# Kernel optimization log

Hardware: AMD Instinct MI355X
Metric: run time of the kernel (lower is better)

Reference implementation:

```python
import jax, jax.numpy as jnp
import numpy as np


def setup_inputs() -> dict:
    key = jax.random.key(0)
    ks = jax.random.split(key, 10)
    B, T = 256, 256
    num_q, dk, dv, C = 1000, 128, 128, 32
    xn_k = (2.0 / (dk + C)) ** 0.5   # xavier_normal for Mk
    xn_v = (2.0 / (C + dv)) ** 0.5   # xavier_normal for Mv
    return dict(
        skills=jax.random.randint(ks[0], (B, T), 0, num_q),
        responses=jax.random.randint(ks[1], (B, T), 0, 2),
        k_emb=jax.random.normal(ks[2], (num_q, dk), dtype=jnp.float32) * 0.05,
        v_emb=jax.random.normal(ks[3], (2 * num_q, dv), dtype=jnp.float32) * 0.05,
        Mk=jax.random.normal(ks[4], (dk, C), dtype=jnp.float32) * xn_k,
        Mv0=jax.random.normal(ks[5], (C, dv), dtype=jnp.float32) * xn_v,
        f_W=jax.random.normal(ks[6], (2 * dk, dk), dtype=jnp.float32) * 0.05,
        f_b=jnp.zeros((dk,), jnp.float32),
        p_W=jax.random.normal(ks[7], (dk, 1), dtype=jnp.float32) * 0.05,
        p_b=jnp.zeros((1,), jnp.float32),
        e_W=jax.random.normal(ks[8], (dv, dv), dtype=jnp.float32) * 0.05,
        e_b=jnp.zeros((dv,), jnp.float32),
        a_W=jax.random.normal(ks[9], (dv, dv), dtype=jnp.float32) * 0.05,
        a_b=jnp.zeros((dv,), jnp.float32),
    )


def reference(skills, responses, k_emb, v_emb, Mk, Mv0, f_W, f_b,
              p_W, p_b, e_W, e_b, a_W, a_b):
    num_q = k_emb.shape[0]
    B = skills.shape[0]
    masked_r = responses * (responses > -1).astype(responses.dtype)
    qr = skills + num_q * masked_r
    kt_all = k_emb[skills]   # (B, T, dk)
    vt_all = v_emb[qr]       # (B, T, dv)
    Mvt0 = jnp.broadcast_to(Mv0[None], (B,) + Mv0.shape)  # (B, C, dv)

    def step(Mvt, xs):
        kt, vt = xs                                      # (B,dk), (B,dv)
        wt = jax.nn.softmax(kt @ Mk, axis=-1)            # (B, C) read weights
        rt = jnp.einsum('bc,bcd->bd', wt, Mvt)           # memory read
        ft = jnp.tanh(jnp.concatenate([rt, kt], axis=-1) @ f_W + f_b)
        pt = jax.nn.sigmoid(ft @ p_W + p_b)[:, 0]        # (B,)
        et = jax.nn.sigmoid(vt @ e_W + e_b)              # erase gate
        at = jnp.tanh(vt @ a_W + a_b)                    # add vector
        Mvt = Mvt * (1.0 - wt[:, :, None] * et[:, None, :]) \
              + wt[:, :, None] * at[:, None, :]
        return Mvt, pt

    xs = (jnp.swapaxes(kt_all, 0, 1), jnp.swapaxes(vt_all, 0, 1))  # time-major
    _, p = jax.lax.scan(step, Mvt0, xs)                  # (T, B)
    p = jnp.swapaxes(p, 0, 1)                            # (B, T)
    pred = p[:, :-1]
    true = responses[:, 1:].astype(jnp.float32)
    return pred, true
```

## Files before the change

kernel.cpp:

```cpp
#include <hip/hip_runtime.h>
#include <math.h>

#define BB 256
#define TT 256
#define NQ 1000
#define DK 128
#define DV 128
#define CC 32

typedef short s16x8 __attribute__((ext_vector_type(8)));
typedef float f32x4 __attribute__((ext_vector_type(4)));
typedef float f32x2 __attribute__((ext_vector_type(2)));

__device__ __forceinline__ float fast_sigmoid(float x) {
    x = fminf(fmaxf(x, -30.f), 30.f);
    return 1.f / (1.f + __expf(-x));
}
__device__ __forceinline__ float fast_tanh(float x) {
    x = fminf(fmaxf(x, -15.f), 15.f);
    float t = __expf(2.f * x);
    return (t - 1.f) / (t + 1.f);
}
__device__ __forceinline__ unsigned short f2bf(float f) {
    unsigned u = __float_as_uint(f);
    u += 0x7fffu + ((u >> 16) & 1u);
    return (unsigned short)(u >> 16);
}
__device__ __forceinline__ float bf2f(unsigned short h) {
    return __uint_as_float((unsigned)h << 16);
}
__device__ __forceinline__ unsigned u4get(uint4 v, int i) {
    return i == 0 ? v.x : i == 1 ? v.y : i == 2 ? v.z : v.w;
}
__device__ __forceinline__ f32x2 mk2(float x, float y) { f32x2 r; r.x = x; r.y = y; return r; }
__device__ __forceinline__ f32x2 fma2(f32x2 a, f32x2 b, f32x2 c) {
    return __builtin_elementwise_fma(a, b, c);
}

__global__ __launch_bounds__(256) void conv_kernel(
    const float* __restrict__ eW, const float* __restrict__ aW,
    const float* __restrict__ fW, const float* __restrict__ Mk,
    unsigned short* __restrict__ eWt, unsigned short* __restrict__ aWt,
    unsigned short* __restrict__ fWat, unsigned short* __restrict__ fWbt,
    unsigned short* __restrict__ Mkt)
{
    int idx = blockIdx.x * 256 + threadIdx.x;
    if (idx < 16384) {
        int n = idx >> 7, k = idx & 127;
        eWt[idx] = f2bf(eW[k * 128 + n]);
    } else if (idx < 32768) {
        int i = idx - 16384; int n = i >> 7, k = i & 127;
        aWt[i] = f2bf(aW[k * 128 + n]);
    } else if (idx < 49152) {
        int i = idx - 32768; int n = i >> 7, k = i & 127;
        fWat[i] = f2bf(fW[k * 128 + n]);
    } else if (idx < 65536) {
        int i = idx - 49152; int n = i >> 7, k = i & 127;
        fWbt[i] = f2bf(fW[(128 + k) * 128 + n]);
    } else if (idx < 69632) {
        int i = idx - 65536; int n = i >> 7, k = i & 127;
        Mkt[i] = f2bf(Mk[k * 32 + n]);
    }
}

template <int NT, class F>
__device__ __forceinline__ void mfma_phase(const unsigned short* Wlds,
                                           const s16x8 (&aF)[4], int lane, F emit)
{
    const int quad = lane >> 4, nrow = lane & 15;
#pragma unroll
    for (int nt = 0; nt < NT; ++nt) {
        f32x4 acc = {0.f, 0.f, 0.f, 0.f};
#pragma unroll
        for (int kb = 0; kb < 4; ++kb) {
            s16x8 bf = *(const s16x8*)&Wlds[(nt * 16 + nrow) * 136 + kb * 32 + quad * 8];
            acc = __builtin_amdgcn_mfma_f32_16x16x32_bf16(aF[kb], bf, acc, 0, 0, 0);
        }
        int col = nt * 16 + nrow;
        emit(quad * 4 + 0, col, acc[0]);
        emit(quad * 4 + 1, col, acc[1]);
        emit(quad * 4 + 2, col, acc[2]);
        emit(quad * 4 + 3, col, acc[3]);
    }
}

__global__ __launch_bounds__(256) void pre_kernel(
    const int* __restrict__ skills, const int* __restrict__ responses,
    const float* __restrict__ k_emb, const float* __restrict__ v_emb,
    const float* __restrict__ fb, const float* __restrict__ eb,
    const float* __restrict__ ab,
    const unsigned short* __restrict__ Mkt, const unsigned short* __restrict__ fWbt,
    const unsigned short* __restrict__ eWt, const unsigned short* __restrict__ aWt,
    float* __restrict__ Wo, unsigned* __restrict__ EA,
    unsigned short* __restrict__ Ko, float* __restrict__ outTrue,
    int t0, int Tc)
{
    const int tid = threadIdx.x;
    const int lane = tid & 63;
    const int m_base = (tid >> 6) * 16;
    const int mrow = lane & 15, quad = lane >> 4;
    const size_t base = (size_t)blockIdx.x * 64;

    __shared__ __align__(16) unsigned short Albs[64 * 136];
    __shared__ __align__(16) unsigned short Wlds[128 * 136];
    __shared__ float lg[64 * 33];
    __shared__ int sIdx[64], qIdx[64];

    if (tid < 64) {
        int flat = (int)base + tid;
        int b = flat / Tc, tcc = flat % Tc;
        int t = t0 + tcc;
        int gi = b * TT + t;
        int s = skills[gi];
        int r = responses[gi];
        sIdx[tid] = s;
        qIdx[tid] = s + NQ * ((r > -1) ? r : 0);
        if (t >= 1) outTrue[b * (TT - 1) + (t - 1)] = (float)r;
    }
    __syncthreads();

    {
        int row = tid >> 2, c0 = (tid & 3) * 32;
        int s = sIdx[row];
        const float* src = k_emb + (size_t)s * DK + c0;
#pragma unroll
        for (int j = 0; j < 8; ++j) {
            float4 v = *(const float4*)(src + j * 4);
            unsigned short* dp = &Albs[row * 136 + c0 + j * 4];
            dp[0] = f2bf(v.x); dp[1] = f2bf(v.y); dp[2] = f2bf(v.z); dp[3] = f2bf(v.w);
        }
        int n = tid >> 3, k0 = (tid & 7) * 16;
        *(s16x8*)&Wlds[n * 136 + k0]     = *(const s16x8*)&Mkt[n * 128 + k0];
        *(s16x8*)&Wlds[n * 136 + k0 + 8] = *(const s16x8*)&Mkt[n * 128 + k0 + 8];
    }
    __syncthreads();

    s16x8 aF[4];
#pragma unroll
    for (int kb = 0; kb < 4; ++kb)
        aF[kb] = *(const s16x8*)&Albs[(m_base + mrow) * 136 + kb * 32 + quad * 8];
    mfma_phase<2>(Wlds, aF, lane, [&](int ml, int col, float x) {
        lg[(m_base + ml) * 33 + col] = x;
    });
    __syncthreads();

    {
        int n = tid >> 1, k0 = (tid & 1) * 64;
#pragma unroll
        for (int j = 0; j < 8; ++j)
            *(s16x8*)&Wlds[n * 136 + k0 + j * 8] = *(const s16x8*)&fWbt[n * 128 + k0 + j * 8];
    }
    if (tid < 64) {
        float m = -1e30f;
#pragma unroll
        for (int c = 0; c < CC; ++c) m = fmaxf(m, lg[tid * 33 + c]);
        float ex[CC]; float sum = 0.f;
#pragma unroll
        for (int c = 0; c < CC; ++c) { ex[c] = __expf(lg[tid * 33 + c] - m); sum += ex[c]; }
        float inv = 1.f / sum;
        float* wp = Wo + (base + tid) * CC;
#pragma unroll
        for (int c = 0; c < CC; c += 4)
            *(float4*)(wp + c) = make_float4(ex[c] * inv, ex[c + 1] * inv,
                                             ex[c + 2] * inv, ex[c + 3] * inv);
    }
    __syncthreads();

    mfma_phase<8>(Wlds, aF, lane, [&](int ml, int col, float x) {
        size_t r = base + m_base + ml;
        Ko[r * 128 + col] = f2bf(x + fb[col]);
    });
    __syncthreads();

    {
        int row = tid >> 2, c0 = (tid & 3) * 32;
        int q = qIdx[row];
        const float* src = v_emb + (size_t)q * DV + c0;
#pragma unroll
        for (int j = 0; j < 8; ++j) {
            float4 v = *(const float4*)(src + j * 4);
            unsigned short* dp = &Albs[row * 136 + c0 + j * 4];
            dp[0] = f2bf(v.x); dp[1] = f2bf(v.y); dp[2] = f2bf(v.z); dp[3] = f2bf(v.w);
        }
        int n = tid >> 1, k0 = (tid & 1) * 64;
#pragma unroll
        for (int j = 0; j < 8; ++j)
            *(s16x8*)&Wlds[n * 136 + k0 + j * 8] = *(const s16x8*)&eWt[n * 128 + k0 + j * 8];
    }
    __syncthreads();

#pragma unroll
    for (int kb = 0; kb < 4; ++kb)
        aF[kb] = *(const s16x8*)&Albs[(m_base + mrow) * 136 + kb * 32 + quad * 8];
    mfma_phase<8>(Wlds, aF, lane, [&](int ml, int col, float x) {
        Albs[(m_base + ml) * 136 + col] = f2bf(fast_sigmoid(x + eb[col]));
    });
    __syncthreads();

    {
        int n = tid >> 1, k0 = (tid & 1) * 64;
#pragma unroll
        for (int j = 0; j < 8; ++j)
            *(s16x8*)&Wlds[n * 136 + k0 + j * 8] = *(const s16x8*)&aWt[n * 128 + k0 + j * 8];
    }
    __syncthreads();

    mfma_phase<8>(Wlds, aF, lane, [&](int ml, int col, float x) {
        size_t r = base + m_base + ml;
        int bb = (int)(r / (size_t)Tc);
        int t  = (int)(r - (size_t)bb * Tc);
        size_t o4 = (((size_t)bb * (Tc >> 5) + (t >> 5)) * 8 + ((t >> 2) & 7)) * 128 + col;
        unsigned lo = Albs[(m_base + ml) * 136 + col];
        unsigned hi = (unsigned)f2bf(fast_tanh(x + ab[col])) << 16;
        EA[o4 * 4 + (t & 3)] = hi | lo;
    });
}


#define CH 32
#define WROW 36
#define RSTR 136

#define LOAD_W(gg) do {                                                       \
    const float* ws = Wb + (size_t)(gg) * CH * 32;                            \
    wr0 = *(const float4*)(ws + tid * 8);                                     \
    wr1 = *(const float4*)(ws + tid * 8 + 4);                                 \
} while (0)

#define PUB_W(gg) do {                                                        \
    float* wd = &Wl[(gg) & 1][lr * WROW + lq * 8];                            \
    *(float4*)wd = wr0; *(float4*)(wd + 4) = wr1;                             \
} while (0)

#define LOAD_EA(ER, gg) do {                                                  \
    const uint4* src = EA4 + ((size_t)(bq + (gg))) * 1024 + tid;              \
    _Pragma("unroll")                                                         \
    for (int j = 0; j < 8; ++j) ER[j] = src[j * 128];                         \
} while (0)

#define PREF8(A0,A1,A2,A3,A4,A5,A6,A7, rowidx) do {                           \
    const float* _wr = wlc + (rowidx) * WROW;                                 \
    A0 = *(const float4*)(_wr + 0);  A1 = *(const float4*)(_wr + 4);          \
    A2 = *(const float4*)(_wr + 8);  A3 = *(const float4*)(_wr + 12);         \
    A4 = *(const float4*)(_wr + 16); A5 = *(const float4*)(_wr + 20);         \
    A6 = *(const float4*)(_wr + 24); A7 = *(const float4*)(_wr + 28);         \
} while (0)

#define STEP8(A0,A1,A2,A3,A4,A5,A6,A7, ER, tl) do {                           \
    f32x2 w2[16];                                                             \
    w2[0]  = mk2(A0.x, A0.y); w2[1]  = mk2(A0.z, A0.w);                       \
    w2[2]  = mk2(A1.x, A1.y); w2[3]  = mk2(A1.z, A1.w);                       \
    w2[4]  = mk2(A2.x, A2.y); w2[5]  = mk2(A2.z, A2.w);                       \
    w2[6]  = mk2(A3.x, A3.y); w2[7]  = mk2(A3.z, A3.w);                       \
    w2[8]  = mk2(A4.x, A4.y); w2[9]  = mk2(A4.z, A4.w);                       \
    w2[10] = mk2(A5.x, A5.y); w2[11] = mk2(A5.z, A5.w);                       \
    w2[12] = mk2(A6.x, A6.y); w2[13] = mk2(A6.z, A6.w);                       \
    w2[14] = mk2(A7.x, A7.y); w2[15] = mk2(A7.z, A7.w);                       \
    unsigned ea = u4get(ER[(tl) >> 2], (tl) & 3);                             \
    float e = __uint_as_float(ea << 16);                                      \
    float a = __uint_as_float(ea & 0xffff0000u);                              \
    f32x2 ne2 = mk2(-e, -e);                                                  \
    f32x2 a2  = mk2(a, a);                                                    \
    f32x2 r0 = mk2(0.f, 0.f), r1 = r0, r2 = r0, r3 = r0;                      \
    _Pragma("unroll")                                                         \
    for (int q = 0; q < 4; ++q) {                                             \
        r0 = fma2(w2[4*q+0], Mv2[4*q+0], r0);                                 \
        r1 = fma2(w2[4*q+1], Mv2[4*q+1], r1);                                 \
        r2 = fma2(w2[4*q+2], Mv2[4*q+2], r2);                                 \
        r3 = fma2(w2[4*q+3], Mv2[4*q+3], r3);                                 \
    }                                                                         \
    f32x2 rs = (r0 + r1) + (r2 + r3);                                         \
    slp[(tl) * RSTR + tid] = f2bf(rs.x + rs.y);                               \
    _Pragma("unroll")                                                         \
    for (int i = 0; i < 16; ++i)                                              \
        Mv2[i] = fma2(w2[i], fma2(ne2, Mv2[i], a2), Mv2[i]);                  \
} while (0)

#define SEQ_CHUNK(ER, gg, SL) do {                                            \
    const float* wlc = Wl[(gg) & 1];                                          \
    unsigned short* slp = SL;                                                 \
    PREF8(w0,w1,w2_,w3_,w4_,w5_,w6_,w7_, 0);                                  \
    _Pragma("unroll")                                                         \
    for (int tp = 0; tp < 16; ++tp) {                                         \
        PREF8(u0,u1,u2,u3,u4,u5,u6,u7, 2 * tp + 1);                           \
        STEP8(w0,w1,w2_,w3_,w4_,w5_,w6_,w7_, ER, 2 * tp);                     \
        PREF8(w0,w1,w2_,w3_,w4_,w5_,w6_,w7_,                                  \
              (2 * tp + 2 < 32) ? (2 * tp + 2) : 31);                         \
        STEP8(u0,u1,u2,u3,u4,u5,u6,u7, ER, 2 * tp + 1);                       \
    }                                                                         \
} while (0)

__device__ __forceinline__ void consume_chunk(
    int gc, const unsigned short* sl, const unsigned short* fWl,
    int b, int Tc, int t0,
    const unsigned short* __restrict__ Ko, const float* __restrict__ pW,
    float pbv, float* __restrict__ pred, int tid)
{
    const int lane = tid & 63;
    const int cw = (tid >> 6) & 1;
    const int mrow = lane & 15, quad = lane >> 4;
    s16x8 aF[4];
#pragma unroll
    for (int kb = 0; kb < 4; ++kb)
        aF[kb] = *(const s16x8*)&sl[(cw * 16 + mrow) * RSTR + kb * 32 + quad * 8];
    float p0 = 0.f, p1 = 0.f, p2 = 0.f, p3 = 0.f;
    size_t rbase = (size_t)b * Tc + gc * CH + cw * 16 + quad * 4;
#pragma unroll
    for (int nt = 0; nt < 8; ++nt) {
        f32x4 acc = {0.f, 0.f, 0.f, 0.f};
#pragma unroll
        for (int kb = 0; kb < 4; ++kb) {
            s16x8 bf = *(const s16x8*)&fWl[(nt * 16 + mrow) * RSTR + kb * 32 + quad * 8];
            acc = __builtin_amdgcn_mfma_f32_16x16x32_bf16(aF[kb], bf, acc, 0, 0, 0);
        }
        int col = nt * 16 + mrow;
        float pw = pW[col];
        p0 = fmaf(fast_tanh(acc[0] + bf2f(Ko[(rbase + 0) * 128 + col])), pw, p0);
        p1 = fmaf(fast_tanh(acc[1] + bf2f(Ko[(rbase + 1) * 128 + col])), pw, p1);
        p2 = fmaf(fast_tanh(acc[2] + bf2f(Ko[(rbase + 2) * 128 + col])), pw, p2);
        p3 = fmaf(fast_tanh(acc[3] + bf2f(Ko[(rbase + 3) * 128 + col])), pw, p3);
    }
#pragma unroll
    for (int off = 1; off < 16; off <<= 1) {
        p0 += __shfl_xor(p0, off, 64); p1 += __shfl_xor(p1, off, 64);
        p2 += __shfl_xor(p2, off, 64); p3 += __shfl_xor(p3, off, 64);
    }
    if (mrow == 0) {
        int tb = t0 + gc * CH + cw * 16 + quad * 4;
        float ps[4] = {p0, p1, p2, p3};
#pragma unroll
        for (int reg = 0; reg < 4; ++reg) {
            int t = tb + reg;
            if (t < TT - 1) pred[b * (TT - 1) + t] = fast_sigmoid(ps[reg] + pbv);
        }
    }
}

__global__ __launch_bounds__(256, 1) void fused_kernel(
    const float* __restrict__ W, const unsigned* __restrict__ EA,
    const float* __restrict__ Mv0, const unsigned short* __restrict__ Ko,
    const unsigned short* __restrict__ fWat, const float* __restrict__ pW,
    const float* __restrict__ pb,
    float* __restrict__ pred, float* __restrict__ MvWS,
    int t0, int Tc, int doInit, int doSave)
{
    const int b = blockIdx.x;
    const int tid = threadIdx.x;
    const int nch = Tc / CH;

    __shared__ __align__(16) float Wl[2][CH * WROW];
    __shared__ __align__(16) unsigned short rtl[2][CH * RSTR];
    __shared__ __align__(16) unsigned short fWl[128 * RSTR];

    {
        int n = tid >> 1, k0 = (tid & 1) * 64;
#pragma unroll
        for (int j = 0; j < 8; ++j)
            *(s16x8*)&fWl[n * RSTR + k0 + j * 8] = *(const s16x8*)&fWat[n * 128 + k0 + j * 8];
    }

    const int lr = tid >> 2, lq = tid & 3;
    const float* __restrict__ Wb = W + (size_t)b * Tc * 32;
    const uint4* __restrict__ EA4 = (const uint4*)EA;
    const int bq = b * nch;
    f32x2 Mv2[16];
    float4 wr0, wr1;
    float4 w0, w1, w2_, w3_, w4_, w5_, w6_, w7_;
    float4 u0, u1, u2, u3, u4, u5, u6, u7;
    uint4 erA[8], erB[8];
    float pbv = 0.f;

    if (tid < 128) {
        if (doInit) {
#pragma unroll
            for (int i = 0; i < 16; ++i)
                Mv2[i] = mk2(Mv0[(2 * i) * 128 + tid], Mv0[(2 * i + 1) * 128 + tid]);
        } else {
#pragma unroll
            for (int i = 0; i < 16; ++i)
                Mv2[i] = mk2(MvWS[(size_t)b * 4096 + (2 * i) * 128 + tid],
                             MvWS[(size_t)b * 4096 + (2 * i + 1) * 128 + tid]);
        }
        LOAD_W(0); PUB_W(0);
        LOAD_EA(erA, 0);
        if (nch > 1) LOAD_W(1);
    } else {
        pbv = pb[0];
    }
    __syncthreads();

    for (int g = 0; g < nch; g += 2) {
        if (tid < 128) {
            if (g + 1 < nch) PUB_W(g + 1);
            if (g + 2 < nch) LOAD_W(g + 2);
            if (g + 1 < nch) LOAD_EA(erB, g + 1);
            SEQ_CHUNK(erA, g, rtl[0]);
        } else if (g >= 1) {
            consume_chunk(g - 1, rtl[1], fWl, b, Tc, t0, Ko, pW, pbv, pred, tid);
        }
        __syncthreads();

        if (tid < 128) {
            if (g + 1 < nch) {
                if (g + 2 < nch) PUB_W(g + 2);
                if (g + 3 < nch) LOAD_W(g + 3);
                if (g + 2 < nch) LOAD_EA(erA, g + 2);
                SEQ_CHUNK(erB, g + 1, rtl[1]);
            }
        } else {
            consume_chunk(g, rtl[0], fWl, b, Tc, t0, Ko, pW, pbv, pred, tid);
        }
        __syncthreads();
    }
    if (!(nch & 1) && tid >= 128) {
        consume_chunk(nch - 1, rtl[1], fWl, b, Tc, t0, Ko, pW, pbv, pred, tid);
    }

    if (doSave && tid < 128) {
#pragma unroll
        for (int i = 0; i < 16; ++i) {
            MvWS[(size_t)b * 4096 + (2 * i) * 128 + tid]     = Mv2[i].x;
            MvWS[(size_t)b * 4096 + (2 * i + 1) * 128 + tid] = Mv2[i].y;
        }
    }
}


extern "C" void kernel_launch(void* const* d_in, const int* in_sizes, int n_in,
                              void* d_out, int out_size, void* d_ws, size_t ws_size,
                              hipStream_t stream) {
    const int*   skills    = (const int*)d_in[0];
    const int*   responses = (const int*)d_in[1];
    const float* k_emb     = (const float*)d_in[2];
    const float* v_emb     = (const float*)d_in[3];
    const float* Mk        = (const float*)d_in[4];
    const float* Mv0       = (const float*)d_in[5];
    const float* f_W       = (const float*)d_in[6];
    const float* f_b       = (const float*)d_in[7];
    const float* p_W       = (const float*)d_in[8];
    const float* p_b       = (const float*)d_in[9];
    const float* e_W       = (const float*)d_in[10];
    const float* e_b       = (const float*)d_in[11];
    const float* a_W       = (const float*)d_in[12];
    const float* a_b       = (const float*)d_in[13];

    float* pred    = (float*)d_out;
    float* outTrue = pred + BB * (TT - 1);

    int Tc = TT;
    for (;;) {
        size_t need = (size_t)BB * Tc * 896 + 69632 * 2;
        if (Tc < TT) need += (size_t)BB * 4096 * 4;
        if (need <= ws_size || Tc <= 32) break;
        Tc >>= 1;
    }

    char* p = (char*)d_ws;
    float* Wo = (float*)p;                     p += (size_t)BB * Tc * 32 * 4;
    unsigned* EA = (unsigned*)p;               p += (size_t)BB * Tc * 128 * 4;
    unsigned short* Ko = (unsigned short*)p;   p += (size_t)BB * Tc * 128 * 2;
    unsigned short* eWt = (unsigned short*)p;  p += 16384 * 2;
    unsigned short* aWt = (unsigned short*)p;  p += 16384 * 2;
    unsigned short* fWat = (unsigned short*)p; p += 16384 * 2;
    unsigned short* fWbt = (unsigned short*)p; p += 16384 * 2;
    unsigned short* Mkt = (unsigned short*)p;  p += 4096 * 2;
    float* MvWS = (float*)p;

    conv_kernel<<<272, 256, 0, stream>>>(e_W, a_W, f_W, Mk,
                                         eWt, aWt, fWat, fWbt, Mkt);

    for (int t0 = 0; t0 < TT; t0 += Tc) {
        pre_kernel<<<(BB * Tc) / 64, 256, 0, stream>>>(
            skills, responses, k_emb, v_emb, f_b, e_b, a_b,
            Mkt, fWbt, eWt, aWt, Wo, EA, Ko, outTrue, t0, Tc);
        fused_kernel<<<BB, 256, 0, stream>>>(
            Wo, EA, Mv0, Ko, fWat, p_W, p_b, pred, MvWS,
            t0, Tc, t0 == 0 ? 1 : 0, (t0 + Tc < TT) ? 1 : 0);
    }
}
```

Baseline: 174.0 us.

## Load embeddings straight into MFMA fragments and fuse softmax via shuffles in pre_kernel

The pre-kernel stops staging gathered k/v embedding rows through shared memory and loads them directly from global memory into bf16 MFMA A-fragments. The read-weight softmax is now computed in registers with cross-lane shuffles, which removes the logits shared buffer and several barriers. The erase-gate results stay in registers to be packed together with the add vector, and sched_barriers are placed around the prefetches in the recurrent loop to pin their position. This raises register pressure and makes the global gathers less coalesced, and the sched barriers may constrain the compiler's scheduling.

```diff
diff --git a/kernel.cpp b/kernel.cpp
--- a/kernel.cpp
+++ b/kernel.cpp
@@ -35,6 +35,14 @@
 __device__ __forceinline__ f32x2 mk2(float x, float y) { f32x2 r; r.x = x; r.y = y; return r; }
 __device__ __forceinline__ f32x2 fma2(f32x2 a, f32x2 b, f32x2 c) {
     return __builtin_elementwise_fma(a, b, c);
+}
+__device__ __forceinline__ s16x8 cvt8(float4 v0, float4 v1) {
+    s16x8 f;
+    f[0] = (short)f2bf(v0.x); f[1] = (short)f2bf(v0.y);
+    f[2] = (short)f2bf(v0.z); f[3] = (short)f2bf(v0.w);
+    f[4] = (short)f2bf(v1.x); f[5] = (short)f2bf(v1.y);
+    f[6] = (short)f2bf(v1.z); f[7] = (short)f2bf(v1.w);
+    return f;
 }
 
 __global__ __launch_bounds__(256) void conv_kernel(
@@ -63,27 +71,6 @@
     }
 }
 
-template <int NT, class F>
-__device__ __forceinline__ void mfma_phase(const unsigned short* Wlds,
-                                           const s16x8 (&aF)[4], int lane, F emit)
-{
-    const int quad = lane >> 4, nrow = lane & 15;
-#pragma unroll
-    for (int nt = 0; nt < NT; ++nt) {
-        f32x4 acc = {0.f, 0.f, 0.f, 0.f};
-#pragma unroll
-        for (int kb = 0; kb < 4; ++kb) {
-            s16x8 bf = *(const s16x8*)&Wlds[(nt * 16 + nrow) * 136 + kb * 32 + quad * 8];
-            acc = __builtin_amdgcn_mfma_f32_16x16x32_bf16(aF[kb], bf, acc, 0, 0, 0);
-        }
-        int col = nt * 16 + nrow;
-        emit(quad * 4 + 0, col, acc[0]);
-        emit(quad * 4 + 1, col, acc[1]);
-        emit(quad * 4 + 2, col, acc[2]);
-        emit(quad * 4 + 3, col, acc[3]);
-    }
-}
-
 __global__ __launch_bounds__(256) void pre_kernel(
     const int* __restrict__ skills, const int* __restrict__ responses,
     const float* __restrict__ k_emb, const float* __restrict__ v_emb,
@@ -101,47 +88,60 @@
     const int mrow = lane & 15, quad = lane >> 4;
     const size_t base = (size_t)blockIdx.x * 64;
 
-    __shared__ __align__(16) unsigned short Albs[64 * 136];
     __shared__ __align__(16) unsigned short Wlds[128 * 136];
-    __shared__ float lg[64 * 33];
-    __shared__ int sIdx[64], qIdx[64];
-
-    if (tid < 64) {
-        int flat = (int)base + tid;
-        int b = flat / Tc, tcc = flat % Tc;
-        int t = t0 + tcc;
-        int gi = b * TT + t;
-        int s = skills[gi];
-        int r = responses[gi];
-        sIdx[tid] = s;
-        qIdx[tid] = s + NQ * ((r > -1) ? r : 0);
-        if (t >= 1) outTrue[b * (TT - 1) + (t - 1)] = (float)r;
-    }
-    __syncthreads();
-
-    {
-        int row = tid >> 2, c0 = (tid & 3) * 32;
-        int s = sIdx[row];
-        const float* src = k_emb + (size_t)s * DK + c0;
-#pragma unroll
-        for (int j = 0; j < 8; ++j) {
-            float4 v = *(const float4*)(src + j * 4);
-            unsigned short* dp = &Albs[row * 136 + c0 + j * 4];
-            dp[0] = f2bf(v.x); dp[1] = f2bf(v.y); dp[2] = f2bf(v.z); dp[3] = f2bf(v.w);
-        }
+
+    int grow = (int)base + m_base + mrow;
+    int gb = grow / Tc;
+    int gt = t0 + (grow - gb * Tc);
+    int gi = gb * TT + gt;
+    int s = skills[gi];
+    int r = responses[gi];
+    int q = s + NQ * ((r > -1) ? r : 0);
+    if (quad == 0 && gt >= 1) outTrue[gb * (TT - 1) + (gt - 1)] = (float)r;
+
+    {
         int n = tid >> 3, k0 = (tid & 7) * 16;
         *(s16x8*)&Wlds[n * 136 + k0]     = *(const s16x8*)&Mkt[n * 128 + k0];
         *(s16x8*)&Wlds[n * 136 + k0 + 8] = *(const s16x8*)&Mkt[n * 128 + k0 + 8];
     }
-    __syncthreads();
 
     s16x8 aF[4];
-#pragma unroll
-    for (int kb = 0; kb < 4; ++kb)
-        aF[kb] = *(const s16x8*)&Albs[(m_base + mrow) * 136 + kb * 32 + quad * 8];
-    mfma_phase<2>(Wlds, aF, lane, [&](int ml, int col, float x) {
-        lg[(m_base + ml) * 33 + col] = x;
-    });
+    {
+        const float* kr = k_emb + (size_t)s * DK + quad * 8;
+#pragma unroll
+        for (int kb = 0; kb < 4; ++kb)
+            aF[kb] = cvt8(*(const float4*)(kr + kb * 32),
+                          *(const float4*)(kr + kb * 32 + 4));
+    }
+    __syncthreads();
+
+    {
+        f32x4 l0 = {0.f, 0.f, 0.f, 0.f}, l1 = {0.f, 0.f, 0.f, 0.f};
+#pragma unroll
+        for (int kb = 0; kb < 4; ++kb) {
+            s16x8 b0 = *(const s16x8*)&Wlds[mrow * 136 + kb * 32 + quad * 8];
+            s16x8 b1 = *(const s16x8*)&Wlds[(16 + mrow) * 136 + kb * 32 + quad * 8];
+            l0 = __builtin_amdgcn_mfma_f32_16x16x32_bf16(aF[kb], b0, l0, 0, 0, 0);
+            l1 = __builtin_amdgcn_mfma_f32_16x16x32_bf16(aF[kb], b1, l1, 0, 0, 0);
+        }
+#pragma unroll
+        for (int reg = 0; reg < 4; ++reg) {
+            float a0 = l0[reg], a1 = l1[reg];
+            float m = fmaxf(a0, a1);
+#pragma unroll
+            for (int off = 1; off < 16; off <<= 1)
+                m = fmaxf(m, __shfl_xor(m, off, 64));
+            float e0 = __expf(a0 - m), e1 = __expf(a1 - m);
+            float ssum = e0 + e1;
+#pragma unroll
+            for (int off = 1; off < 16; off <<= 1)
+                ssum += __shfl_xor(ssum, off, 64);
+            float inv = 1.f / ssum;
+            size_t rowg = base + m_base + quad * 4 + reg;
+            Wo[rowg * 32 + mrow]      = e0 * inv;
+            Wo[rowg * 32 + 16 + mrow] = e1 * inv;
+        }
+    }
     __syncthreads();
 
     {
@@ -150,38 +150,36 @@
         for (int j = 0; j < 8; ++j)
             *(s16x8*)&Wlds[n * 136 + k0 + j * 8] = *(const s16x8*)&fWbt[n * 128 + k0 + j * 8];
     }
-    if (tid < 64) {
-        float m = -1e30f;
-#pragma unroll
-        for (int c = 0; c < CC; ++c) m = fmaxf(m, lg[tid * 33 + c]);
-        float ex[CC]; float sum = 0.f;
-#pragma unroll
-        for (int c = 0; c < CC; ++c) { ex[c] = __expf(lg[tid * 33 + c] - m); sum += ex[c]; }
-        float inv = 1.f / sum;
-        float* wp = Wo + (base + tid) * CC;
-#pragma unroll
-        for (int c = 0; c < CC; c += 4)
-            *(float4*)(wp + c) = make_float4(ex[c] * inv, ex[c + 1] * inv,
-                                             ex[c + 2] * inv, ex[c + 3] * inv);
-    }
-    __syncthreads();
-
-    mfma_phase<8>(Wlds, aF, lane, [&](int ml, int col, float x) {
-        size_t r = base + m_base + ml;
-        Ko[r * 128 + col] = f2bf(x + fb[col]);
-    });
-    __syncthreads();
-
-    {
-        int row = tid >> 2, c0 = (tid & 3) * 32;
-        int q = qIdx[row];
-        const float* src = v_emb + (size_t)q * DV + c0;
-#pragma unroll
-        for (int j = 0; j < 8; ++j) {
-            float4 v = *(const float4*)(src + j * 4);
-            unsigned short* dp = &Albs[row * 136 + c0 + j * 4];
-            dp[0] = f2bf(v.x); dp[1] = f2bf(v.y); dp[2] = f2bf(v.z); dp[3] = f2bf(v.w);
-        }
+    __syncthreads();
+
+    s16x8 vF[4];
+    {
+        const float* vr = v_emb + (size_t)q * DV + quad * 8;
+#pragma unroll
+        for (int kb = 0; kb < 4; ++kb)
+            vF[kb] = cvt8(*(const float4*)(vr + kb * 32),
+                          *(const float4*)(vr + kb * 32 + 4));
+    }
+
+#pragma unroll
+    for (int nt = 0; nt < 8; ++nt) {
+        f32x4 acc = {0.f, 0.f, 0.f, 0.f};
+#pragma unroll
+        for (int kb = 0; kb < 4; ++kb) {
+            s16x8 bf = *(const s16x8*)&Wlds[(nt * 16 + mrow) * 136 + kb * 32 + quad * 8];
+            acc = __builtin_amdgcn_mfma_f32_16x16x32_bf16(aF[kb], bf, acc, 0, 0, 0);
+        }
+        int col = nt * 16 + mrow;
+        float fbv = fb[col];
+#pragma unroll
+        for (int reg = 0; reg < 4; ++reg) {
+            size_t rr = base + m_base + quad * 4 + reg;
+            Ko[rr * 128 + col] = f2bf(acc[reg] + fbv);
+        }
+    }
+    __syncthreads();
+
+    {
         int n = tid >> 1, k0 = (tid & 1) * 64;
 #pragma unroll
         for (int j = 0; j < 8; ++j)
@@ -189,12 +187,21 @@
     }
     __syncthreads();
 
-#pragma unroll
-    for (int kb = 0; kb < 4; ++kb)
-        aF[kb] = *(const s16x8*)&Albs[(m_base + mrow) * 136 + kb * 32 + quad * 8];
-    mfma_phase<8>(Wlds, aF, lane, [&](int ml, int col, float x) {
-        Albs[(m_base + ml) * 136 + col] = f2bf(fast_sigmoid(x + eb[col]));
-    });
+    float etr[8][4];
+#pragma unroll
+    for (int nt = 0; nt < 8; ++nt) {
+        f32x4 acc = {0.f, 0.f, 0.f, 0.f};
+#pragma unroll
+        for (int kb = 0; kb < 4; ++kb) {
+            s16x8 bf = *(const s16x8*)&Wlds[(nt * 16 + mrow) * 136 + kb * 32 + quad * 8];
+            acc = __builtin_amdgcn_mfma_f32_16x16x32_bf16(vF[kb], bf, acc, 0, 0, 0);
+        }
+        int col = nt * 16 + mrow;
+        float ebv = eb[col];
+#pragma unroll
+        for (int reg = 0; reg < 4; ++reg)
+            etr[nt][reg] = fast_sigmoid(acc[reg] + ebv);
+    }
     __syncthreads();
 
     {
@@ -205,21 +212,34 @@
     }
     __syncthreads();
 
-    mfma_phase<8>(Wlds, aF, lane, [&](int ml, int col, float x) {
-        size_t r = base + m_base + ml;
-        int bb = (int)(r / (size_t)Tc);
-        int t  = (int)(r - (size_t)bb * Tc);
-        size_t o4 = (((size_t)bb * (Tc >> 5) + (t >> 5)) * 8 + ((t >> 2) & 7)) * 128 + col;
-        unsigned lo = Albs[(m_base + ml) * 136 + col];
-        unsigned hi = (unsigned)f2bf(fast_tanh(x + ab[col])) << 16;
-        EA[o4 * 4 + (t & 3)] = hi | lo;
-    });
+#pragma unroll
+    for (int nt = 0; nt < 8; ++nt) {
+        f32x4 acc = {0.f, 0.f, 0.f, 0.f};
+#pragma unroll
+        for (int kb = 0; kb < 4; ++kb) {
+            s16x8 bf = *(const s16x8*)&Wlds[(nt * 16 + mrow) * 136 + kb * 32 + quad * 8];
+            acc = __builtin_amdgcn_mfma_f32_16x16x32_bf16(vF[kb], bf, acc, 0, 0, 0);
+        }
+        int col = nt * 16 + mrow;
+        float abv = ab[col];
+#pragma unroll
+        for (int reg = 0; reg < 4; ++reg) {
+            size_t rr = base + m_base + quad * 4 + reg;
+            int bb = (int)(rr / (size_t)Tc);
+            int t  = (int)(rr - (size_t)bb * Tc);
+            size_t o4 = (((size_t)bb * (Tc >> 5) + (t >> 5)) * 8 + ((t >> 2) & 7)) * 128 + col;
+            unsigned lo = f2bf(etr[nt][reg]);
+            unsigned hi = (unsigned)f2bf(fast_tanh(acc[reg] + abv)) << 16;
+            EA[o4 * 4 + (t & 3)] = hi | lo;
+        }
+    }
 }
 
 
 #define CH 32
 #define WROW 36
 #define RSTR 136
+#define SB() __builtin_amdgcn_sched_barrier(0)
 
 #define LOAD_W(gg) do {                                                       \
     const float* ws = Wb + (size_t)(gg) * CH * 32;                            \
@@ -282,10 +302,10 @@
     PREF8(w0,w1,w2_,w3_,w4_,w5_,w6_,w7_, 0);                                  \
     _Pragma("unroll")                                                         \
     for (int tp = 0; tp < 16; ++tp) {                                         \
-        PREF8(u0,u1,u2,u3,u4,u5,u6,u7, 2 * tp + 1);                           \
+        SB(); PREF8(u0,u1,u2,u3,u4,u5,u6,u7, 2 * tp + 1); SB();               \
         STEP8(w0,w1,w2_,w3_,w4_,w5_,w6_,w7_, ER, 2 * tp);                     \
-        PREF8(w0,w1,w2_,w3_,w4_,w5_,w6_,w7_,                                  \
-              (2 * tp + 2 < 32) ? (2 * tp + 2) : 31);                         \
+        SB(); PREF8(w0,w1,w2_,w3_,w4_,w5_,w6_,w7_,                            \
+                    (2 * tp + 2 < 32) ? (2 * tp + 2) : 31); SB();             \
         STEP8(u0,u1,u2,u3,u4,u5,u6,u7, ER, 2 * tp + 1);                       \
     }                                                                         \
 } while (0)
```

Result: faster. 165.0 us, median of 2 (-5.2%).
